# Kernel optimization log

Hardware: AMD Instinct MI355X
Metric: run time of the kernel (lower is better)

The kernel has to match this reference:

```python
import jax, jax.numpy as jnp
import numpy as np

N_NODES = 100000
N_EDGES = 1600000
F_IN = 128
F_OUT = 32


def setup_inputs() -> dict:
    key = jax.random.key(0)
    k1, k2, k3 = jax.random.split(key, 3)
    x = jax.random.normal(k1, (N_NODES, F_IN), dtype=jnp.float32)
    edge_index = jax.random.randint(k2, (2, N_EDGES), 0, N_NODES, dtype=jnp.int64)
    # Glorot-style init for the GCNConv linear weight [F_IN, F_OUT]
    W = jax.random.normal(k3, (F_IN, F_OUT), dtype=jnp.float32) * (1.0 / np.sqrt(F_IN))
    b = jnp.zeros((F_OUT,), dtype=jnp.float32)
    return {"x": x, "edge_index": edge_index, "W": W, "b": b}


def reference(x, edge_index, W, b):
    N = x.shape[0]
    # --- add self loops (PyG GCNConv default) ---
    loops = jnp.arange(N, dtype=edge_index.dtype)
    src = jnp.concatenate([edge_index[0], loops])  # message sources j
    dst = jnp.concatenate([edge_index[1], loops])  # aggregation targets i
    # --- symmetric normalization: deg^-1/2[src] * deg^-1/2[dst] ---
    ones = jnp.ones(src.shape[0], dtype=x.dtype)
    deg = jax.ops.segment_sum(ones, dst, num_segments=N)  # in-degree incl. self loop
    dinv = jnp.where(deg > 0, jax.lax.rsqrt(deg), jnp.zeros_like(deg))
    norm = dinv[src] * dinv[dst]  # [E+N]
    # --- linear transform then gather-scale-scatter aggregate ---
    h = x @ W  # [N, F_OUT]
    msgs = h[src] * norm[:, None]  # [E+N, F_OUT]
    out = jax.ops.segment_sum(msgs, dst, num_segments=N)  # [N, F_OUT]
    return out + b
```

## Files before the change

### kernel.cpp

```cpp
#include <hip/hip_runtime.h>
#include <hip/hip_fp16.h>

#define N_NODES 100000
#define N_EDGES 1600000
#define F_IN    128
#define F_OUT   32

#define BKT_SHIFT  7
#define BKT_SIZE   128
#define NBKT       782
#define BKT_STRIDE 2560
#define BIN_TILE   4096
#define EPT        16
#define NTILES     ((N_EDGES + BIN_TILE - 1) / BIN_TILE)

typedef _Float16 f16x8 __attribute__((ext_vector_type(8)));
typedef float    f32x4 __attribute__((ext_vector_type(4)));

__global__ void init_kernel(int* __restrict__ gcur) {
    int i = blockIdx.x * blockDim.x + threadIdx.x;
    if (i < NBKT) gcur[i] = 0;
}

__global__ __launch_bounds__(256) void bin_kernel(const int* __restrict__ ei,
                                                  int* __restrict__ gcur,
                                                  unsigned int* __restrict__ binned) {
    __shared__ int cnt[NBKT], pos[NBKT], gbase[NBKT];
    int t = threadIdx.x;
    for (int b = t; b < NBKT; b += 256) { cnt[b] = 0; pos[b] = 0; }
    __syncthreads();
    int ebase = blockIdx.x * BIN_TILE;
    unsigned int pk[EPT];
    short bkt[EPT];
#pragma unroll
    for (int k = 0; k < EPT; ++k) {
        int e = ebase + k * 256 + t;
        if (e < N_EDGES) {
            int s = ei[e];
            int d = ei[N_EDGES + e];
            bkt[k] = (short)(d >> BKT_SHIFT);
            pk[k]  = (unsigned)s | ((unsigned)(d & (BKT_SIZE - 1)) << 25);
            atomicAdd(&cnt[bkt[k]], 1);
        } else {
            bkt[k] = -1;
        }
    }
    __syncthreads();
    for (int b = t; b < NBKT; b += 256)
        if (cnt[b] > 0) gbase[b] = atomicAdd(&gcur[b], cnt[b]);
    __syncthreads();
#pragma unroll
    for (int k = 0; k < EPT; ++k) {
        if (bkt[k] >= 0) {
            int r = atomicAdd(&pos[bkt[k]], 1);
            int p = gbase[bkt[k]] + r;
            if (p < BKT_STRIDE)
                binned[(size_t)bkt[k] * BKT_STRIDE + p] = pk[k];
        }
    }
}

__global__ __launch_bounds__(256) void dinv_from_bins_kernel(const unsigned int* __restrict__ binned,
                                                             const int* __restrict__ gcur,
                                                             float* __restrict__ dinv) {
    __shared__ int cnt[BKT_SIZE];
    int t = threadIdx.x;
    int b = blockIdx.x;
    if (t < BKT_SIZE) cnt[t] = 0;
    __syncthreads();
    int ne = gcur[b];
    if (ne > BKT_STRIDE) ne = BKT_STRIDE;
    const unsigned int* eb = binned + (size_t)b * BKT_STRIDE;
    for (int i = t; i < ne; i += 256)
        atomicAdd(&cnt[eb[i] >> 25], 1);
    __syncthreads();
    int gnode = b * BKT_SIZE + t;
    if (t < BKT_SIZE && gnode < N_NODES)
        dinv[gnode] = rsqrtf((float)(cnt[t] + 1));
}

#define WH_STRIDE 136
__global__ __launch_bounds__(256) void matmul_kernel(const float4* __restrict__ x4,
                                                     const float* __restrict__ W,
                                                     const float* __restrict__ dinv,
                                                     __half* __restrict__ hs) {
    __shared__ _Float16 Wh[F_OUT * WH_STRIDE];
    int t = threadIdx.x;
    {
        int col = t & 31, kb = (t >> 5) * 16;
        for (int u = 0; u < 16; ++u)
            Wh[col * WH_STRIDE + kb + u] = (_Float16)W[(kb + u) * F_OUT + col];
    }
    __syncthreads();

    int w = t >> 6, l = t & 63;
    int lr = l & 15, kg = l >> 4;
    int row = blockIdx.x * 64 + w * 16 + lr;
    const float4* xr = x4 + (size_t)row * 32;
    bool rok = row < N_NODES;

    f16x8 a[4];
#pragma unroll
    for (int ks = 0; ks < 4; ++ks) {
        float4 v0, v1;
        if (rok) {
            v0 = xr[ks * 8 + kg * 2];
            v1 = xr[ks * 8 + kg * 2 + 1];
        } else {
            v0 = make_float4(0, 0, 0, 0);
            v1 = v0;
        }
        f16x8 av;
        av[0] = (_Float16)v0.x; av[1] = (_Float16)v0.y;
        av[2] = (_Float16)v0.z; av[3] = (_Float16)v0.w;
        av[4] = (_Float16)v1.x; av[5] = (_Float16)v1.y;
        av[6] = (_Float16)v1.z; av[7] = (_Float16)v1.w;
        a[ks] = av;
    }

    f32x4 c0 = {0.f, 0.f, 0.f, 0.f}, c1 = {0.f, 0.f, 0.f, 0.f};
#pragma unroll
    for (int ks = 0; ks < 4; ++ks) {
        f16x8 b0 = *(const f16x8*)&Wh[lr * WH_STRIDE + ks * 32 + kg * 8];
        f16x8 b1 = *(const f16x8*)&Wh[(16 + lr) * WH_STRIDE + ks * 32 + kg * 8];
        c0 = __builtin_amdgcn_mfma_f32_16x16x32_f16(a[ks], b0, c0, 0, 0, 0);
        c1 = __builtin_amdgcn_mfma_f32_16x16x32_f16(a[ks], b1, c1, 0, 0, 0);
    }

    int orow0 = blockIdx.x * 64 + w * 16 + kg * 4;
#pragma unroll
    for (int i = 0; i < 4; ++i) {
        int orow = orow0 + i;
        if (orow < N_NODES) {
            float dv = dinv[orow];
            hs[(size_t)orow * F_OUT + lr]      = (__half)(c0[i] * dv);
            hs[(size_t)orow * F_OUT + 16 + lr] = (__half)(c1[i] * dv);
        }
    }
}

__device__ inline void acc4(uint2 u, float& a0, float& a1, float& a2, float& a3) {
    float2 f0 = __half22float2(*(__half2*)&u.x);
    float2 f1 = __half22float2(*(__half2*)&u.y);
    a0 += f0.x; a1 += f0.y; a2 += f1.x; a3 += f1.y;
}

__global__ __launch_bounds__(256) void aggregate_kernel(const unsigned int* __restrict__ binned,
                                                        const int* __restrict__ gcur,
                                                        const uint2* __restrict__ hs4,
                                                        const float* __restrict__ dinv,
                                                        const float* __restrict__ bias,
                                                        float* __restrict__ out) {
    __shared__ int scan[BKT_SIZE];
    __shared__ int rp[BKT_SIZE + 1];
    __shared__ int cur[BKT_SIZE];
    __shared__ int se[BKT_STRIDE];
    int t = threadIdx.x;
    int b = blockIdx.x;
    int ne = gcur[b];
    if (ne > BKT_STRIDE) ne = BKT_STRIDE;
    const unsigned int* eb = binned + (size_t)b * BKT_STRIDE;

    if (t < BKT_SIZE) scan[t] = 0;
    __syncthreads();
    for (int i = t; i < ne; i += 256)
        atomicAdd(&scan[eb[i] >> 25], 1);
    __syncthreads();
    int v = (t < BKT_SIZE) ? scan[t] : 0;
    for (int off = 1; off < BKT_SIZE; off <<= 1) {
        int add = (t < BKT_SIZE && t >= off) ? scan[t - off] : 0;
        __syncthreads();
        if (t < BKT_SIZE) scan[t] += add;
        __syncthreads();
    }
    if (t < BKT_SIZE) {
        int ex = scan[t] - v;
        rp[t] = ex;
        cur[t] = ex;
    }
    if (t == 0) rp[BKT_SIZE] = ne;
    __syncthreads();
    for (int i = t; i < ne; i += 256) {
        unsigned pk = eb[i];
        int dl = (int)(pk >> 25);
        int r = atomicAdd(&cur[dl], 1);
        se[r] = (int)(pk & 0x1FFFFFF);
    }
    __syncthreads();

    int slot = t >> 3, j4 = t & 7;
    float4 bv = *(const float4*)&bias[j4 * 4];
    for (int n = slot; n < BKT_SIZE; n += 32) {
        int gnode = b * BKT_SIZE + n;
        if (gnode >= N_NODES) break;
        int beg = rp[n], end = rp[n + 1];
        float a0 = 0.f, a1 = 0.f, a2 = 0.f, a3 = 0.f;
        int p = beg;
        for (; p + 7 < end; p += 8) {
            uint2 u0 = hs4[(size_t)se[p]     * 8 + j4];
            uint2 u1 = hs4[(size_t)se[p + 1] * 8 + j4];
            uint2 u2 = hs4[(size_t)se[p + 2] * 8 + j4];
            uint2 u3 = hs4[(size_t)se[p + 3] * 8 + j4];
            uint2 u4 = hs4[(size_t)se[p + 4] * 8 + j4];
            uint2 u5 = hs4[(size_t)se[p + 5] * 8 + j4];
            uint2 u6 = hs4[(size_t)se[p + 6] * 8 + j4];
            uint2 u7 = hs4[(size_t)se[p + 7] * 8 + j4];
            acc4(u0, a0, a1, a2, a3); acc4(u1, a0, a1, a2, a3);
            acc4(u2, a0, a1, a2, a3); acc4(u3, a0, a1, a2, a3);
            acc4(u4, a0, a1, a2, a3); acc4(u5, a0, a1, a2, a3);
            acc4(u6, a0, a1, a2, a3); acc4(u7, a0, a1, a2, a3);
        }
        for (; p + 3 < end; p += 4) {
            uint2 u0 = hs4[(size_t)se[p]     * 8 + j4];
            uint2 u1 = hs4[(size_t)se[p + 1] * 8 + j4];
            uint2 u2 = hs4[(size_t)se[p + 2] * 8 + j4];
            uint2 u3 = hs4[(size_t)se[p + 3] * 8 + j4];
            acc4(u0, a0, a1, a2, a3); acc4(u1, a0, a1, a2, a3);
            acc4(u2, a0, a1, a2, a3); acc4(u3, a0, a1, a2, a3);
        }
        for (; p < end; ++p) {
            uint2 u0 = hs4[(size_t)se[p] * 8 + j4];
            acc4(u0, a0, a1, a2, a3);
        }
        float dv = dinv[gnode];
        uint2 us = hs4[(size_t)gnode * 8 + j4];
        float2 s0 = __half22float2(*(__half2*)&us.x);
        float2 s1 = __half22float2(*(__half2*)&us.y);
        float4 o;
        o.x = bv.x + dv * (a0 + s0.x);
        o.y = bv.y + dv * (a1 + s0.y);
        o.z = bv.z + dv * (a2 + s1.x);
        o.w = bv.w + dv * (a3 + s1.y);
        *(float4*)&out[(size_t)gnode * F_OUT + j4 * 4] = o;
    }
}

extern "C" void kernel_launch(void* const* d_in, const int* in_sizes, int n_in,
                              void* d_out, int out_size, void* d_ws, size_t ws_size,
                              hipStream_t stream) {
    const float* x  = (const float*)d_in[0];
    const int*   ei = (const int*)d_in[1];
    const float* W  = (const float*)d_in[2];
    const float* b  = (const float*)d_in[3];
    float* out = (float*)d_out;

    int*          gcur   = (int*)d_ws;
    unsigned int* binned = (unsigned int*)(gcur + 1024);
    float*        dinv   = (float*)(binned + (size_t)NBKT * BKT_STRIDE);
    __half*       hs     = (__half*)(dinv + ((N_NODES + 3) & ~3));

    const int B = 256;

    init_kernel<<<1, 1024, 0, stream>>>(gcur);

    bin_kernel<<<NTILES, B, 0, stream>>>(ei, gcur, binned);

    dinv_from_bins_kernel<<<NBKT, B, 0, stream>>>(binned, gcur, dinv);

    matmul_kernel<<<(N_NODES + 63) / 64, B, 0, stream>>>((const float4*)x, W, dinv, hs);

    aggregate_kernel<<<NBKT, B, 0, stream>>>(binned, gcur, (const uint2*)hs, dinv, b, out);
}
```

Baseline: 76.77 us.

## Split each aggregation bucket across four blocks of 32 nodes

The aggregate kernel now launches four blocks per 128-node bucket, each owning a 32-node sub-range. Every block loads the whole bucket's edge list into registers once, then counts and scatters only the edges for its own sub-range into a smaller shared buffer. Each thread group handles a single node, so the per-block node loop goes away. This raises block count and occupancy and shrinks shared memory per block, at the cost of reading each bucket's edge list four times and adding a clamp on per-sub-range edges.

```diff
diff --git a/kernel.cpp b/kernel.cpp
--- a/kernel.cpp
+++ b/kernel.cpp
@@ -13,6 +13,10 @@
 #define BIN_TILE   4096
 #define EPT        16
 #define NTILES     ((N_EDGES + BIN_TILE - 1) / BIN_TILE)
+
+#define AGG_SPLIT  4
+#define SUB        32
+#define SUB_STRIDE 768
 
 typedef _Float16 f16x8 __attribute__((ext_vector_type(8)));
 typedef float    f32x4 __attribute__((ext_vector_type(4)));
@@ -151,88 +155,109 @@
                                                         const float* __restrict__ dinv,
                                                         const float* __restrict__ bias,
                                                         float* __restrict__ out) {
-    __shared__ int scan[BKT_SIZE];
-    __shared__ int rp[BKT_SIZE + 1];
-    __shared__ int cur[BKT_SIZE];
-    __shared__ int se[BKT_STRIDE];
-    int t = threadIdx.x;
-    int b = blockIdx.x;
+    __shared__ int scan[SUB];
+    __shared__ int rp[SUB + 1];
+    __shared__ int cur[SUB];
+    __shared__ int se[SUB_STRIDE];
+    int t = threadIdx.x;
+    int b   = blockIdx.x >> 2;
+    int sub = blockIdx.x & 3;
     int ne = gcur[b];
     if (ne > BKT_STRIDE) ne = BKT_STRIDE;
     const unsigned int* eb = binned + (size_t)b * BKT_STRIDE;
 
-    if (t < BKT_SIZE) scan[t] = 0;
-    __syncthreads();
-    for (int i = t; i < ne; i += 256)
-        atomicAdd(&scan[eb[i] >> 25], 1);
-    __syncthreads();
-    int v = (t < BKT_SIZE) ? scan[t] : 0;
-    for (int off = 1; off < BKT_SIZE; off <<= 1) {
-        int add = (t < BKT_SIZE && t >= off) ? scan[t - off] : 0;
+    if (t < SUB) scan[t] = 0;
+    __syncthreads();
+
+    unsigned pk[10];
+#pragma unroll
+    for (int k = 0; k < 10; ++k) {
+        int i = t + k * 256;
+        pk[k] = (i < ne) ? eb[i] : 0xFFFFFFFFu;
+    }
+#pragma unroll
+    for (int k = 0; k < 10; ++k) {
+        if (pk[k] != 0xFFFFFFFFu) {
+            int dl = (int)(pk[k] >> 25);
+            if ((dl >> 5) == sub) atomicAdd(&scan[dl & 31], 1);
+        }
+    }
+    __syncthreads();
+    int v = (t < SUB) ? scan[t] : 0;
+    for (int off = 1; off < SUB; off <<= 1) {
+        int add = (t < SUB && t >= off) ? scan[t - off] : 0;
         __syncthreads();
-        if (t < BKT_SIZE) scan[t] += add;
+        if (t < SUB) scan[t] += add;
         __syncthreads();
     }
-    if (t < BKT_SIZE) {
+    if (t < SUB) {
         int ex = scan[t] - v;
+        if (ex > SUB_STRIDE) ex = SUB_STRIDE;
         rp[t] = ex;
         cur[t] = ex;
     }
-    if (t == 0) rp[BKT_SIZE] = ne;
-    __syncthreads();
-    for (int i = t; i < ne; i += 256) {
-        unsigned pk = eb[i];
-        int dl = (int)(pk >> 25);
-        int r = atomicAdd(&cur[dl], 1);
-        se[r] = (int)(pk & 0x1FFFFFF);
-    }
-    __syncthreads();
-
-    int slot = t >> 3, j4 = t & 7;
+    if (t == 0) rp[SUB] = (scan[SUB - 1] < SUB_STRIDE) ? 0 : SUB_STRIDE;
+    __syncthreads();
+    if (t == 0) {
+        int tot = scan[SUB - 1];
+        rp[SUB] = (tot > SUB_STRIDE) ? SUB_STRIDE : tot;
+    }
+    __syncthreads();
+#pragma unroll
+    for (int k = 0; k < 10; ++k) {
+        if (pk[k] != 0xFFFFFFFFu) {
+            int dl = (int)(pk[k] >> 25);
+            if ((dl >> 5) == sub) {
+                int r = atomicAdd(&cur[dl & 31], 1);
+                if (r < SUB_STRIDE) se[r] = (int)(pk[k] & 0x1FFFFFF);
+            }
+        }
+    }
+    __syncthreads();
+
+    int n = t >> 3, j4 = t & 7;
+    int gnode = b * BKT_SIZE + sub * SUB + n;
+    if (gnode >= N_NODES) return;
     float4 bv = *(const float4*)&bias[j4 * 4];
-    for (int n = slot; n < BKT_SIZE; n += 32) {
-        int gnode = b * BKT_SIZE + n;
-        if (gnode >= N_NODES) break;
-        int beg = rp[n], end = rp[n + 1];
-        float a0 = 0.f, a1 = 0.f, a2 = 0.f, a3 = 0.f;
-        int p = beg;
-        for (; p + 7 < end; p += 8) {
-            uint2 u0 = hs4[(size_t)se[p]     * 8 + j4];
-            uint2 u1 = hs4[(size_t)se[p + 1] * 8 + j4];
-            uint2 u2 = hs4[(size_t)se[p + 2] * 8 + j4];
-            uint2 u3 = hs4[(size_t)se[p + 3] * 8 + j4];
-            uint2 u4 = hs4[(size_t)se[p + 4] * 8 + j4];
-            uint2 u5 = hs4[(size_t)se[p + 5] * 8 + j4];
-            uint2 u6 = hs4[(size_t)se[p + 6] * 8 + j4];
-            uint2 u7 = hs4[(size_t)se[p + 7] * 8 + j4];
-            acc4(u0, a0, a1, a2, a3); acc4(u1, a0, a1, a2, a3);
-            acc4(u2, a0, a1, a2, a3); acc4(u3, a0, a1, a2, a3);
-            acc4(u4, a0, a1, a2, a3); acc4(u5, a0, a1, a2, a3);
-            acc4(u6, a0, a1, a2, a3); acc4(u7, a0, a1, a2, a3);
-        }
-        for (; p + 3 < end; p += 4) {
-            uint2 u0 = hs4[(size_t)se[p]     * 8 + j4];
-            uint2 u1 = hs4[(size_t)se[p + 1] * 8 + j4];
-            uint2 u2 = hs4[(size_t)se[p + 2] * 8 + j4];
-            uint2 u3 = hs4[(size_t)se[p + 3] * 8 + j4];
-            acc4(u0, a0, a1, a2, a3); acc4(u1, a0, a1, a2, a3);
-            acc4(u2, a0, a1, a2, a3); acc4(u3, a0, a1, a2, a3);
-        }
-        for (; p < end; ++p) {
-            uint2 u0 = hs4[(size_t)se[p] * 8 + j4];
-            acc4(u0, a0, a1, a2, a3);
-        }
-        float dv = dinv[gnode];
-        uint2 us = hs4[(size_t)gnode * 8 + j4];
-        float2 s0 = __half22float2(*(__half2*)&us.x);
-        float2 s1 = __half22float2(*(__half2*)&us.y);
-        float4 o;
-        o.x = bv.x + dv * (a0 + s0.x);
-        o.y = bv.y + dv * (a1 + s0.y);
-        o.z = bv.z + dv * (a2 + s1.x);
-        o.w = bv.w + dv * (a3 + s1.y);
-        *(float4*)&out[(size_t)gnode * F_OUT + j4 * 4] = o;
-    }
+    int beg = rp[n], end = rp[n + 1];
+    float a0 = 0.f, a1 = 0.f, a2 = 0.f, a3 = 0.f;
+    int p = beg;
+    for (; p + 7 < end; p += 8) {
+        uint2 u0 = hs4[(size_t)se[p]     * 8 + j4];
+        uint2 u1 = hs4[(size_t)se[p + 1] * 8 + j4];
+        uint2 u2 = hs4[(size_t)se[p + 2] * 8 + j4];
+        uint2 u3 = hs4[(size_t)se[p + 3] * 8 + j4];
+        uint2 u4 = hs4[(size_t)se[p + 4] * 8 + j4];
+        uint2 u5 = hs4[(size_t)se[p + 5] * 8 + j4];
+        uint2 u6 = hs4[(size_t)se[p + 6] * 8 + j4];
+        uint2 u7 = hs4[(size_t)se[p + 7] * 8 + j4];
+        acc4(u0, a0, a1, a2, a3); acc4(u1, a0, a1, a2, a3);
+        acc4(u2, a0, a1, a2, a3); acc4(u3, a0, a1, a2, a3);
+        acc4(u4, a0, a1, a2, a3); acc4(u5, a0, a1, a2, a3);
+        acc4(u6, a0, a1, a2, a3); acc4(u7, a0, a1, a2, a3);
+    }
+    for (; p + 3 < end; p += 4) {
+        uint2 u0 = hs4[(size_t)se[p]     * 8 + j4];
+        uint2 u1 = hs4[(size_t)se[p + 1] * 8 + j4];
+        uint2 u2 = hs4[(size_t)se[p + 2] * 8 + j4];
+        uint2 u3 = hs4[(size_t)se[p + 3] * 8 + j4];
+        acc4(u0, a0, a1, a2, a3); acc4(u1, a0, a1, a2, a3);
+        acc4(u2, a0, a1, a2, a3); acc4(u3, a0, a1, a2, a3);
+    }
+    for (; p < end; ++p) {
+        uint2 u0 = hs4[(size_t)se[p] * 8 + j4];
+        acc4(u0, a0, a1, a2, a3);
+    }
+    float dv = dinv[gnode];
+    uint2 us = hs4[(size_t)gnode * 8 + j4];
+    float2 s0 = __half22float2(*(__half2*)&us.x);
+    float2 s1 = __half22float2(*(__half2*)&us.y);
+    float4 o;
+    o.x = bv.x + dv * (a0 + s0.x);
+    o.y = bv.y + dv * (a1 + s0.y);
+    o.z = bv.z + dv * (a2 + s1.x);
+    o.w = bv.w + dv * (a3 + s1.y);
+    *(float4*)&out[(size_t)gnode * F_OUT + j4 * 4] = o;
 }
 
 extern "C" void kernel_launch(void* const* d_in, const int* in_sizes, int n_in,
@@ -259,5 +284,5 @@
 
     matmul_kernel<<<(N_NODES + 63) / 64, B, 0, stream>>>((const float4*)x, W, dinv, hs);
 
-    aggregate_kernel<<<NBKT, B, 0, stream>>>(binned, gcur, (const uint2*)hs, dinv, b, out);
-}
+    aggregate_kernel<<<NBKT * AGG_SPLIT, B, 0, stream>>>(binned, gcur, (const uint2*)hs, dinv, b, out);
+}
```

Result: faster. 75.13 us (-2.1%).
